# Performance work log

Measured on AMD Instinct MI355X. Metric: run time of the kernel, lower is better.

## Reference

```python
import jax, jax.numpy as jnp
import numpy as np

N_NODES = 100000
N_EDGES = 3200000
N_FEAT = 16
N_GRAPHS = 1024


def setup_inputs() -> dict:
    key = jax.random.key(0)
    ks = jax.random.split(key, 12)
    x = jax.random.normal(ks[0], (N_NODES, N_FEAT), dtype=jnp.float32)
    edge_index = jax.random.randint(ks[1], (2, N_EDGES), 0, N_NODES, dtype=jnp.int32)
    batch = jnp.sort(jax.random.randint(ks[2], (N_NODES,), 0, N_GRAPHS, dtype=jnp.int32))
    def lin(k, fan_in, fan_out):
        s = 1.0 / np.sqrt(fan_in)
        return jax.random.uniform(k, (fan_in, fan_out), jnp.float32, -s, s)
    W1 = lin(ks[3], N_FEAT, 64); b1 = jnp.zeros((64,), jnp.float32)
    W2 = lin(ks[4], 64, 32);     b2 = jnp.zeros((32,), jnp.float32)
    fc1_W = lin(ks[5], 32, 16);  fc1_b = jnp.zeros((16,), jnp.float32)
    fc2_W = lin(ks[6], 16, 1);   fc2_b = jnp.zeros((1,), jnp.float32)
    return {"x": x, "edge_index": edge_index, "batch": batch,
            "W1": W1, "b1": b1, "W2": W2, "b2": b2,
            "fc1_W": fc1_W, "fc1_b": fc1_b, "fc2_W": fc2_W, "fc2_b": fc2_b}


def _gcn_conv(h, W, b, src, dst, norm, n_nodes):
    # h: [N, Fin] -> [N, Fout]; symmetric-normalized scatter-add (PyG GCNConv)
    h = h @ W
    msg = h[src] * norm[:, None]            # edge-wise gather + scale
    out = jax.ops.segment_sum(msg, dst, num_segments=n_nodes)
    return out + b


def reference(x, edge_index, batch, W1, b1, W2, b2, fc1_W, fc1_b, fc2_W, fc2_b):
    n_nodes = x.shape[0]
    # add self-loops
    loops = jnp.arange(n_nodes, dtype=edge_index.dtype)
    src = jnp.concatenate([edge_index[0], loops])
    dst = jnp.concatenate([edge_index[1], loops])
    deg = jax.ops.segment_sum(jnp.ones_like(dst, dtype=x.dtype), dst, num_segments=n_nodes)
    dinv = jnp.where(deg > 0, jax.lax.rsqrt(deg), 0.0)
    norm = dinv[src] * dinv[dst]

    h = jax.nn.relu(_gcn_conv(x, W1, b1, src, dst, norm, n_nodes))
    # dropout p=0.2 is identity at inference
    h = jax.nn.relu(_gcn_conv(h, W2, b2, src, dst, norm, n_nodes))

    # global mean pool over graphs
    sums = jax.ops.segment_sum(h, batch, num_segments=N_GRAPHS)
    cnts = jax.ops.segment_sum(jnp.ones((n_nodes,), h.dtype), batch, num_segments=N_GRAPHS)
    g = sums / jnp.maximum(cnts, 1.0)[:, None]

    g = jax.nn.relu(g @ fc1_W + fc1_b)
    # dropout p=0.5 is identity at inference
    out = g @ fc2_W + fc2_b
    return jax.nn.sigmoid(out)  # [N_GRAPHS, 1]
```

## Files before the change

### kernel.cpp

```cpp
#include <hip/hip_runtime.h>
#include <math.h>

#define NNODES  100000
#define NEDGES  3200000
#define NGRAPHS 1024
#define BNODES  196
#define NBUCK   ((NNODES + BNODES - 1) / BNODES)
#define SCAP    8192
#define PADCAP  10240
#define SLDS    7168
#define DUMMY   NNODES
#define CHUNK   4096
#define NCHUNKS ((NEDGES + CHUNK - 1) / CHUNK)

typedef int iv4 __attribute__((ext_vector_type(4)));
typedef float fv2 __attribute__((ext_vector_type(2)));

#if defined(__has_builtin)
#if __has_builtin(__builtin_amdgcn_cvt_pk_f32_fp8) && __has_builtin(__builtin_amdgcn_cvt_pk_fp8_f32)
#define HW_FP8 1
#endif
#endif

__device__ __forceinline__ unsigned bf16pair(float a, float b) {
    unsigned ua = __float_as_uint(a), ub = __float_as_uint(b);
    ua += 0x7fffu + ((ua >> 16) & 1u);
    ub += 0x7fffu + ((ub >> 16) & 1u);
    return (ua >> 16) | (ub & 0xffff0000u);
}
__device__ __forceinline__ float bflo(unsigned u) { return __uint_as_float(u << 16); }
__device__ __forceinline__ float bfhi(unsigned u) { return __uint_as_float(u & 0xffff0000u); }

__device__ __forceinline__ unsigned fp8_of(float v) {
    unsigned s = (__float_as_uint(v) >> 24) & 0x80u;
    float a = fminf(fabsf(v), 448.f);
    unsigned ub = __float_as_uint(a);
    unsigned lsb = (ub >> 20) & 1u;
    ub += 0x0007FFFFu + lsb;
    int em = (int)(ub >> 20) - (120 << 3);
    if (em < 1) return s;
    if (em > 0x7E) em = 0x7E;
    return s | (unsigned)em;
}
__device__ __forceinline__ float fp8_to_f(unsigned b) {
    unsigned em = b & 0x7Fu;
    unsigned s = (b & 0x80u) << 24;
    float f = __uint_as_float(s | ((em + 0x3C0u) << 20));
    return (em >= 8u) ? f : 0.f;
}
__device__ __forceinline__ unsigned fp8x4_pack(float a, float b, float c, float d) {
    a = fminf(fmaxf(a, -448.f), 448.f);
    b = fminf(fmaxf(b, -448.f), 448.f);
    c = fminf(fmaxf(c, -448.f), 448.f);
    d = fminf(fmaxf(d, -448.f), 448.f);
#ifdef HW_FP8
    int w = __builtin_amdgcn_cvt_pk_fp8_f32(a, b, 0, false);
    w = __builtin_amdgcn_cvt_pk_fp8_f32(c, d, w, true);
    return (unsigned)w;
#else
    return fp8_of(a) | (fp8_of(b) << 8) | (fp8_of(c) << 16) | (fp8_of(d) << 24);
#endif
}
__device__ __forceinline__ fv2 f8lo(unsigned w) {
#ifdef HW_FP8
    return __builtin_amdgcn_cvt_pk_f32_fp8((int)w, false);
#else
    fv2 t; t.x = fp8_to_f(w & 0xFFu); t.y = fp8_to_f((w >> 8) & 0xFFu); return t;
#endif
}
__device__ __forceinline__ fv2 f8hi(unsigned w) {
#ifdef HW_FP8
    return __builtin_amdgcn_cvt_pk_f32_fp8((int)w, true);
#else
    fv2 t; t.x = fp8_to_f((w >> 16) & 0xFFu); t.y = fp8_to_f(w >> 24); return t;
#endif
}


__global__ void zero4_kernel(int4* p, int nvec) {
    int i = blockIdx.x * blockDim.x + threadIdx.x;
    if (i < nvec) p[i] = make_int4(0, 0, 0, 0);
}


__global__ void binA_kernel(const int* __restrict__ src, const int* __restrict__ dst,
                            int* __restrict__ bucketCur, int* __restrict__ stage) {
    __shared__ int lcnt[NBUCK + 1];
    __shared__ int boff[NBUCK + 1];
    __shared__ int gbase[NBUCK + 1];
    __shared__ int cur[NBUCK + 1];
    __shared__ int wtot[4];
    __shared__ int packed[CHUNK];
    __shared__ unsigned short bof[CHUNK];
    int tid = threadIdx.x;
    int beg = blockIdx.x * CHUNK;
    int end = beg + CHUNK; if (end > NEDGES) end = NEDGES;
    int cnt = end - beg;

    for (int i = tid; i <= NBUCK; i += 256) lcnt[i] = 0;
    __syncthreads();

    int ent[16];
    int bk[16];
#pragma unroll
    for (int it = 0; it < 4; ++it) {
        int e0 = beg + tid * 4 + it * 1024;
        if (e0 < end) {
            iv4 d4 = __builtin_nontemporal_load((const iv4*)(dst + e0));
            iv4 s4 = __builtin_nontemporal_load((const iv4*)(src + e0));
            int b;
            b = d4.x / BNODES; ent[it*4+0] = s4.x | ((d4.x - b*BNODES) << 17); bk[it*4+0] = b; atomicAdd(&lcnt[b], 1);
            b = d4.y / BNODES; ent[it*4+1] = s4.y | ((d4.y - b*BNODES) << 17); bk[it*4+1] = b; atomicAdd(&lcnt[b], 1);
            b = d4.z / BNODES; ent[it*4+2] = s4.z | ((d4.z - b*BNODES) << 17); bk[it*4+2] = b; atomicAdd(&lcnt[b], 1);
            b = d4.w / BNODES; ent[it*4+3] = s4.w | ((d4.w - b*BNODES) << 17); bk[it*4+3] = b; atomicAdd(&lcnt[b], 1);
        } else {
            bk[it*4+0] = -1; bk[it*4+1] = -1; bk[it*4+2] = -1; bk[it*4+3] = -1;
            ent[it*4+0] = 0; ent[it*4+1] = 0; ent[it*4+2] = 0; ent[it*4+3] = 0;
        }
    }
    __syncthreads();

    int b0 = 2 * tid, b1 = 2 * tid + 1;
    int c0 = lcnt[b0];
    int c1 = (b1 < NBUCK) ? lcnt[b1] : 0;
    int sum = c0 + c1;
    int lane = tid & 63, wid = tid >> 6;
    int v = sum;
#pragma unroll
    for (int o = 1; o < 64; o <<= 1) {
        int t = __shfl_up(v, o, 64);
        if (lane >= o) v += t;
    }
    if (lane == 63) wtot[wid] = v;
    __syncthreads();
    int woff = 0;
#pragma unroll
    for (int w = 0; w < 4; ++w) woff += (w < wid) ? wtot[w] : 0;
    int excl = woff + v - sum;
    boff[b0] = excl; cur[b0] = excl;
    if (b1 < NBUCK) { boff[b1] = excl + c0; cur[b1] = excl + c0; }
    if (c0 > 0) gbase[b0] = atomicAdd(&bucketCur[b0], c0);
    if (b1 < NBUCK && c1 > 0) gbase[b1] = atomicAdd(&bucketCur[b1], c1);
    __syncthreads();

#pragma unroll
    for (int k = 0; k < 16; ++k) {
        int b = bk[k];
        if (b >= 0) {
            int p = atomicAdd(&cur[b], 1);
            packed[p] = ent[k];
            bof[p] = (unsigned short)b;
        }
    }
    __syncthreads();

    for (int i = tid; i < cnt; i += 256) {
        int b = bof[i];
        int addr = b * SCAP + gbase[b] + (i - boff[b]);
        stage[addr] = packed[i];
    }
}


__global__ void binB_kernel(const int* __restrict__ bucketCur,
                            const int* __restrict__ stage, const float2* __restrict__ x,
                            int* __restrict__ entries, int* __restrict__ rowptr,
                            int* __restrict__ rowend,
                            float* __restrict__ dinv, unsigned* __restrict__ xs) {
    __shared__ int s[256];
    __shared__ int ncur[256];
    __shared__ float ndinv[256];
    __shared__ int wt[4];
    __shared__ int se[SLDS];
    int b = blockIdx.x;
    int cntE = bucketCur[b];
    int bbase = b * PADCAP;
    int nlo = b * BNODES;
    int nn = NNODES - nlo; if (nn > BNODES) nn = BNODES;
    int sb = b * SCAP;
    int tid = threadIdx.x;

    s[tid] = 0;
    __syncthreads();
    for (int e = tid; e < cntE; e += 256) {
        int w = stage[sb + e];
        if (e < SLDS) se[e] = w;
        atomicAdd(&s[(unsigned)w >> 17], 1);
    }
    __syncthreads();
    int v = s[tid];
    int p16 = (v + 15) & ~15;
    int lane = tid & 63, wid = tid >> 6;
    int iv = p16;
#pragma unroll
    for (int o = 1; o < 64; o <<= 1) {
        int t = __shfl_up(iv, o, 64);
        if (lane >= o) iv += t;
    }
    if (lane == 63) wt[wid] = iv;
    __syncthreads();
    int woff = 0;
#pragma unroll
    for (int w2 = 0; w2 < 4; ++w2) woff += (w2 < wid) ? wt[w2] : 0;
    int pexcl = woff + iv - p16;
    ncur[tid] = pexcl;
    if (tid < nn) {
        rowptr[nlo + tid] = bbase + pexcl;
        rowend[nlo + tid] = bbase + pexcl + p16;
        float di = rsqrtf((float)(v + 1));
        dinv[nlo + tid] = di;
        ndinv[tid] = di;
    }
    __syncthreads();
    for (int i = tid; i < nn * 8; i += 256) {
        int node = i >> 3, w = i & 7;
        float2 v2 = x[(size_t)(nlo + node) * 8 + w];
        float di = ndinv[node];
        xs[(nlo + node) * 8 + w] = bf16pair(v2.x * di, v2.y * di);
    }
    if (b == NBUCK - 1) {
        for (int i = tid; i < 8; i += 256) xs[NNODES * 8 + i] = 0u;
    }
    if (tid < nn) {
        int base = bbase + pexcl;
        for (int j = v; j < p16; ++j) entries[base + j] = DUMMY;
    }
    for (int e = tid; e < cntE; e += 256) {
        unsigned w = (unsigned)((e < SLDS) ? se[e] : stage[sb + e]);
        int dl = (int)(w >> 17);
        int slot = atomicAdd(&ncur[dl], 1);
        entries[bbase + slot] = (int)(w & 0x1FFFFu);
    }
}


__device__ __forceinline__ void acc_bf(unsigned u, fv2& a) {
    fv2 t; t.x = bflo(u); t.y = bfhi(u);
    a += t;
}
#define ACCX4(V) { acc_bf((V).x, acc0); acc_bf((V).y, acc1); acc_bf((V).z, acc2); acc_bf((V).w, acc3); }
#define QRED(a) { a.x += __shfl_xor(a.x, 2); a.y += __shfl_xor(a.y, 2); \
                  a.x += __shfl_xor(a.x, 4); a.y += __shfl_xor(a.y, 4); }

__global__ void __launch_bounds__(256) gatherX_mlp_kernel(const int* __restrict__ entries,
        const int* __restrict__ rowptr, const int* __restrict__ rowend,
        const float* __restrict__ dinv, const uint4* __restrict__ xsv,
        const float* __restrict__ W1, const float* __restrict__ b1,
        const float* __restrict__ W2, unsigned* __restrict__ hm2f) {
    __shared__ __align__(16) float w1s[16 * 64];
    __shared__ __align__(16) float w2s[64 * 32];
    __shared__ float bb1[64];
    int tid = threadIdx.x;
    for (int i = tid; i < 16 * 64; i += 256) w1s[i] = W1[i];
    for (int i = tid; i < 64 * 32; i += 256) w2s[i] = W2[i];
    if (tid < 64) bb1[tid] = b1[tid];
    if (blockIdx.x == 0 && tid < 8) hm2f[NNODES * 8 + tid] = 0u;
    __syncthreads();

    int t = blockIdx.x * 256 + tid;
    int n = t >> 3, lane = t & 7;
    int half = lane & 1, quad = lane >> 1;
    int beg = rowptr[n];
    int nb = (rowend[n] - beg) >> 4;
    fv2 acc0 = {0.f, 0.f}, acc1 = {0.f, 0.f}, acc2 = {0.f, 0.f}, acc3 = {0.f, 0.f};
    if (quad == 0) {
        uint4 sv = xsv[n * 2 + half];
        ACCX4(sv);
    }

    const int* ep = entries + beg + (quad << 2);
    if (nb > 0) {
        uint4 p0, p1, p2, p3;
        iv4 enx = {0, 0, 0, 0};
        {
            iv4 e; __builtin_memcpy(&e, ep, 16);
            p0 = xsv[e.x * 2 + half]; p1 = xsv[e.y * 2 + half];
            p2 = xsv[e.z * 2 + half]; p3 = xsv[e.w * 2 + half];
            if (nb > 1) __builtin_memcpy(&enx, ep + 16, 16);
        }
        for (int i = 1; i < nb; ++i) {
            uint4 c0 = xsv[enx.x * 2 + half], c1 = xsv[enx.y * 2 + half],
                  c2 = xsv[enx.z * 2 + half], c3 = xsv[enx.w * 2 + half];
            if (i + 1 < nb) __builtin_memcpy(&enx, ep + ((i + 1) << 4), 16);
            ACCX4(p0); ACCX4(p1); ACCX4(p2); ACCX4(p3);
            p0 = c0; p1 = c1; p2 = c2; p3 = c3;
        }
        ACCX4(p0); ACCX4(p1); ACCX4(p2); ACCX4(p3);
    }

    QRED(acc0); QRED(acc1); QRED(acc2); QRED(acc3);

    float di = dinv[n];
    float own[8];
    own[0] = acc0.x * di; own[1] = acc0.y * di; own[2] = acc1.x * di; own[3] = acc1.y * di;
    own[4] = acc2.x * di; own[5] = acc2.y * di; own[6] = acc3.x * di; own[7] = acc3.y * di;
    float oth[8];
#pragma unroll
    for (int i2 = 0; i2 < 8; ++i2) oth[i2] = __shfl_xor(own[i2], 1);
    float a16[16];
#pragma unroll
    for (int k = 0; k < 8; ++k) a16[k]     = (half == 0) ? own[k] : oth[k];
#pragma unroll
    for (int k = 0; k < 8; ++k) a16[8 + k] = (half == 0) ? oth[k] : own[k];

    float h[8];
    {
        int j0 = lane * 8;
#pragma unroll
        for (int jj = 0; jj < 8; ++jj) h[jj] = bb1[j0 + jj];
#pragma unroll
        for (int k = 0; k < 16; ++k) {
            const float4* wr = (const float4*)(w1s + k * 64 + j0);
            float4 wa = wr[0], wb = wr[1];
            float av = a16[k];
            h[0] += av * wa.x; h[1] += av * wa.y; h[2] += av * wa.z; h[3] += av * wa.w;
            h[4] += av * wb.x; h[5] += av * wb.y; h[6] += av * wb.z; h[7] += av * wb.w;
        }
#pragma unroll
        for (int jj = 0; jj < 8; ++jj) h[jj] = fmaxf(h[jj], 0.f);
    }

    {
        int j0c = lane * 4;
        float c0 = 0.f, c1 = 0.f, c2 = 0.f, c3 = 0.f;
#pragma unroll
        for (int k = 0; k < 64; ++k) {
            float hv = __shfl(h[k & 7], k >> 3, 8);
            float4 w = *(const float4*)(w2s + k * 32 + j0c);
            c0 += hv * w.x; c1 += hv * w.y; c2 += hv * w.z; c3 += hv * w.w;
        }
        float sc = di * 64.f;
        hm2f[n * 8 + lane] = fp8x4_pack(c0 * sc, c1 * sc, c2 * sc, c3 * sc);
    }
}


#define ACCH4(V) { q0lo += f8lo((V).x); q0hi += f8hi((V).x); \
                   q1lo += f8lo((V).y); q1hi += f8hi((V).y); \
                   q2lo += f8lo((V).z); q2hi += f8hi((V).z); \
                   q3lo += f8lo((V).w); q3hi += f8hi((V).w); }

__global__ void __launch_bounds__(256) gatherH_pool_kernel(const int* __restrict__ entries,
        const int* __restrict__ rowptr, const int* __restrict__ rowend,
        const float* __restrict__ dinv, const uint4* __restrict__ hm4,
        const float4* __restrict__ b2, const int* __restrict__ batch,
        float* __restrict__ psum, float* __restrict__ pcnt) {
    __shared__ float lps[8][32];
    __shared__ float lpc[8];
    int tid = threadIdx.x;
    ((float*)lps)[tid] = 0.f;
    if (tid < 8) lpc[tid] = 0.f;
    __syncthreads();

    int t = blockIdx.x * 256 + tid;
    int n = t >> 3, lane = t & 7;
    int half = lane & 1, quad = lane >> 1;
    int g0 = batch[blockIdx.x * 32];
    int beg = rowptr[n];
    int nb = (rowend[n] - beg) >> 4;
    fv2 q0lo = {0.f,0.f}, q0hi = {0.f,0.f}, q1lo = {0.f,0.f}, q1hi = {0.f,0.f},
        q2lo = {0.f,0.f}, q2hi = {0.f,0.f}, q3lo = {0.f,0.f}, q3hi = {0.f,0.f};
    if (quad == 0) {
        uint4 sv = hm4[n * 2 + half];
        ACCH4(sv);
    }

    const int* ep = entries + beg + (quad << 2);
    if (nb > 0) {
        uint4 p0, p1, p2, p3;
        iv4 enx = {0, 0, 0, 0};
        {
            iv4 e; __builtin_memcpy(&e, ep, 16);
            p0 = hm4[e.x * 2 + half]; p1 = hm4[e.y * 2 + half];
            p2 = hm4[e.z * 2 + half]; p3 = hm4[e.w * 2 + half];
            if (nb > 1) __builtin_memcpy(&enx, ep + 16, 16);
        }
        for (int i = 1; i < nb; ++i) {
            uint4 c0 = hm4[enx.x * 2 + half], c1 = hm4[enx.y * 2 + half],
                  c2 = hm4[enx.z * 2 + half], c3 = hm4[enx.w * 2 + half];
            if (i + 1 < nb) __builtin_memcpy(&enx, ep + ((i + 1) << 4), 16);
            ACCH4(p0); ACCH4(p1); ACCH4(p2); ACCH4(p3);
            p0 = c0; p1 = c1; p2 = c2; p3 = c3;
        }
        ACCH4(p0); ACCH4(p1); ACCH4(p2); ACCH4(p3);
    }

    QRED(q0lo); QRED(q0hi); QRED(q1lo); QRED(q1hi);
    QRED(q2lo); QRED(q2hi); QRED(q3lo); QRED(q3hi);

    if (quad == 0) {
        float sc = dinv[n] * (1.0f / 64.f);
        float4 bv0 = b2[half * 4 + 0], bv1 = b2[half * 4 + 1],
               bv2 = b2[half * 4 + 2], bv3 = b2[half * 4 + 3];
        float vv[16];
        vv[0]  = fmaxf(q0lo.x * sc + bv0.x, 0.f);
        vv[1]  = fmaxf(q0lo.y * sc + bv0.y, 0.f);
        vv[2]  = fmaxf(q0hi.x * sc + bv0.z, 0.f);
        vv[3]  = fmaxf(q0hi.y * sc + bv0.w, 0.f);
        vv[4]  = fmaxf(q1lo.x * sc + bv1.x, 0.f);
        vv[5]  = fmaxf(q1lo.y * sc + bv1.y, 0.f);
        vv[6]  = fmaxf(q1hi.x * sc + bv1.z, 0.f);
        vv[7]  = fmaxf(q1hi.y * sc + bv1.w, 0.f);
        vv[8]  = fmaxf(q2lo.x * sc + bv2.x, 0.f);
        vv[9]  = fmaxf(q2lo.y * sc + bv2.y, 0.f);
        vv[10] = fmaxf(q2hi.x * sc + bv2.z, 0.f);
        vv[11] = fmaxf(q2hi.y * sc + bv2.w, 0.f);
        vv[12] = fmaxf(q3lo.x * sc + bv3.x, 0.f);
        vv[13] = fmaxf(q3lo.y * sc + bv3.y, 0.f);
        vv[14] = fmaxf(q3hi.x * sc + bv3.z, 0.f);
        vv[15] = fmaxf(q3hi.y * sc + bv3.w, 0.f);

        int g = batch[n], gr = g - g0;
        if (gr < 8) {
            float* pg = &lps[gr][half * 16];
#pragma unroll
            for (int k2 = 0; k2 < 16; ++k2) atomicAdd(pg + k2, vv[k2]);
            if (lane == 0) atomicAdd(&lpc[gr], 1.0f);
        } else {
            float* pg = psum + g * 32 + half * 16;
#pragma unroll
            for (int k2 = 0; k2 < 16; ++k2) atomicAdd(pg + k2, vv[k2]);
            if (lane == 0) atomicAdd(&pcnt[g], 1.0f);
        }
    }
    __syncthreads();
    int grf = tid >> 5, f = tid & 31;
    float v = lps[grf][f];
    if (v != 0.f) atomicAdd(&psum[(g0 + grf) * 32 + f], v);
    if (f == 0) {
        float c = lpc[grf];
        if (c != 0.f) atomicAdd(&pcnt[g0 + grf], c);
    }
}


__global__ void head_kernel(const float* __restrict__ psum, const float* __restrict__ pcnt,
                            const float* __restrict__ fc1W, const float* __restrict__ fc1b,
                            const float* __restrict__ fc2W, const float* __restrict__ fc2b,
                            float* __restrict__ out) {
    int g = blockIdx.x * blockDim.x + threadIdx.x;
    if (g >= NGRAPHS) return;
    float inv = 1.0f / fmaxf(pcnt[g], 1.0f);
    float gv[32];
#pragma unroll
    for (int k = 0; k < 32; ++k) gv[k] = psum[g * 32 + k] * inv;
    float o = fc2b[0];
#pragma unroll
    for (int j = 0; j < 16; ++j) {
        float h = fc1b[j];
#pragma unroll
        for (int k = 0; k < 32; ++k) h += gv[k] * fc1W[k * 16 + j];
        h = fmaxf(h, 0.f);
        o += h * fc2W[j];
    }
    out[g] = 1.0f / (1.0f + expf(-o));
}


extern "C" void kernel_launch(void* const* d_in, const int* in_sizes, int n_in,
                              void* d_out, int out_size, void* d_ws, size_t ws_size,
                              hipStream_t stream) {
    const float* x    = (const float*)d_in[0];
    const int*   ei   = (const int*)d_in[1];
    const int*   batch= (const int*)d_in[2];
    const float* W1   = (const float*)d_in[3];
    const float* b1   = (const float*)d_in[4];
    const float* W2   = (const float*)d_in[5];
    const float* b2   = (const float*)d_in[6];
    const float* fc1W = (const float*)d_in[7];
    const float* fc1b = (const float*)d_in[8];
    const float* fc2W = (const float*)d_in[9];
    const float* fc2b = (const float*)d_in[10];
    float* out = (float*)d_out;

    const int* src = ei;
    const int* dst = ei + NEDGES;

    char* wsb = (char*)d_ws;
    int*      bucketCur = (int*)wsb;
    float*    psum      = (float*)(wsb + 2048);
    float*    pcnt      = (float*)(wsb + 133120);
    float*    dinv      = (float*)(wsb + 137216);
    int*      rowptr    = (int*)(wsb + 537216);
    int*      rowend    = (int*)(wsb + 937216);
    int*      stage     = (int*)(wsb + 1337216);
    int*      entries   = (int*)(wsb + 18081664);
    unsigned* xs        = (unsigned*)(wsb + 39012224);
    unsigned* hm2f      = (unsigned*)(wsb + 42212256);

    const int B = 256;
    zero4_kernel<<<(8576 + B - 1) / B, B, 0, stream>>>((int4*)wsb, 8576);

    binA_kernel<<<NCHUNKS, B, 0, stream>>>(src, dst, bucketCur, stage);
    binB_kernel<<<NBUCK, B, 0, stream>>>(bucketCur, stage, (const float2*)x,
                                         entries, rowptr, rowend, dinv, xs);

    const int GTH = NNODES * 8 / B;
    gatherX_mlp_kernel<<<GTH, B, 0, stream>>>(entries, rowptr, rowend, dinv,
                                              (const uint4*)xs, W1, b1, W2, hm2f);
    gatherH_pool_kernel<<<GTH, B, 0, stream>>>(entries, rowptr, rowend, dinv,
                                               (const uint4*)hm2f, (const float4*)b2,
                                               batch, psum, pcnt);
    head_kernel<<<(NGRAPHS + B - 1) / B, B, 0, stream>>>(psum, pcnt, fc1W, fc1b, fc2W, fc2b, out);
}
```

Measured before the change: 231.0 us.

## Halve bucket size and split bucket counters into sub-buckets to cut atomic contention

Buckets now cover 98 nodes instead of 196, giving about 1021 buckets. Each bucket's staging area is split into 4 sub-buckets selected by chunk index, which spreads the global atomicAdd traffic on bucket counters across more addresses. binB then gathers the four sub-regions into LDS, which removes the global-memory fallback for oversized buckets. The cost is more binB blocks doing less work each, with half the threads idle in the per-node phase, and a fixed 1024-entry sub-bucket capacity that could overflow on skewed inputs.

```diff
diff --git a/kernel.cpp b/kernel.cpp
--- a/kernel.cpp
+++ b/kernel.cpp
@@ -4,11 +4,11 @@
 #define NNODES  100000
 #define NEDGES  3200000
 #define NGRAPHS 1024
-#define BNODES  196
+#define BNODES  98
 #define NBUCK   ((NNODES + BNODES - 1) / BNODES)
-#define SCAP    8192
-#define PADCAP  10240
-#define SLDS    7168
+#define NSUB    4
+#define SUBCAP  1024
+#define PADCAP  5120
 #define DUMMY   NNODES
 #define CHUNK   4096
 #define NCHUNKS ((NEDGES + CHUNK - 1) / CHUNK)
@@ -85,19 +85,20 @@
 
 __global__ void binA_kernel(const int* __restrict__ src, const int* __restrict__ dst,
                             int* __restrict__ bucketCur, int* __restrict__ stage) {
-    __shared__ int lcnt[NBUCK + 1];
-    __shared__ int boff[NBUCK + 1];
-    __shared__ int gbase[NBUCK + 1];
-    __shared__ int cur[NBUCK + 1];
+    __shared__ int lcnt[1024];
+    __shared__ int boff[1024];
+    __shared__ int gbase[1024];
+    __shared__ int cur[1024];
     __shared__ int wtot[4];
     __shared__ int packed[CHUNK];
     __shared__ unsigned short bof[CHUNK];
     int tid = threadIdx.x;
+    int sub = blockIdx.x & (NSUB - 1);
     int beg = blockIdx.x * CHUNK;
     int end = beg + CHUNK; if (end > NEDGES) end = NEDGES;
     int cnt = end - beg;
 
-    for (int i = tid; i <= NBUCK; i += 256) lcnt[i] = 0;
+    for (int i = tid; i < 1024; i += 256) lcnt[i] = 0;
     __syncthreads();
 
     int ent[16];
@@ -120,10 +121,9 @@
     }
     __syncthreads();
 
-    int b0 = 2 * tid, b1 = 2 * tid + 1;
-    int c0 = lcnt[b0];
-    int c1 = (b1 < NBUCK) ? lcnt[b1] : 0;
-    int sum = c0 + c1;
+    int q0 = 4 * tid;
+    int c0 = lcnt[q0], c1 = lcnt[q0 + 1], c2 = lcnt[q0 + 2], c3 = lcnt[q0 + 3];
+    int sum = c0 + c1 + c2 + c3;
     int lane = tid & 63, wid = tid >> 6;
     int v = sum;
 #pragma unroll
@@ -137,10 +137,14 @@
 #pragma unroll
     for (int w = 0; w < 4; ++w) woff += (w < wid) ? wtot[w] : 0;
     int excl = woff + v - sum;
-    boff[b0] = excl; cur[b0] = excl;
-    if (b1 < NBUCK) { boff[b1] = excl + c0; cur[b1] = excl + c0; }
-    if (c0 > 0) gbase[b0] = atomicAdd(&bucketCur[b0], c0);
-    if (b1 < NBUCK && c1 > 0) gbase[b1] = atomicAdd(&bucketCur[b1], c1);
+    boff[q0] = excl;     cur[q0] = excl;     excl += c0;
+    boff[q0 + 1] = excl; cur[q0 + 1] = excl; excl += c1;
+    boff[q0 + 2] = excl; cur[q0 + 2] = excl; excl += c2;
+    boff[q0 + 3] = excl; cur[q0 + 3] = excl;
+    if (c0 > 0) gbase[q0]     = atomicAdd(&bucketCur[q0 * NSUB + sub], c0);
+    if (c1 > 0) gbase[q0 + 1] = atomicAdd(&bucketCur[(q0 + 1) * NSUB + sub], c1);
+    if (c2 > 0) gbase[q0 + 2] = atomicAdd(&bucketCur[(q0 + 2) * NSUB + sub], c2);
+    if (c3 > 0) gbase[q0 + 3] = atomicAdd(&bucketCur[(q0 + 3) * NSUB + sub], c3);
     __syncthreads();
 
 #pragma unroll
@@ -156,7 +160,7 @@
 
     for (int i = tid; i < cnt; i += 256) {
         int b = bof[i];
-        int addr = b * SCAP + gbase[b] + (i - boff[b]);
+        int addr = (b * NSUB + sub) * SUBCAP + gbase[b] + (i - boff[b]);
         stage[addr] = packed[i];
     }
 }
@@ -167,49 +171,59 @@
                             int* __restrict__ entries, int* __restrict__ rowptr,
                             int* __restrict__ rowend,
                             float* __restrict__ dinv, unsigned* __restrict__ xs) {
-    __shared__ int s[256];
-    __shared__ int ncur[256];
-    __shared__ float ndinv[256];
-    __shared__ int wt[4];
-    __shared__ int se[SLDS];
+    __shared__ int s[128];
+    __shared__ int ncur[128];
+    __shared__ float ndinv[128];
+    __shared__ int wt[2];
+    __shared__ int se[NSUB * SUBCAP];
     int b = blockIdx.x;
-    int cntE = bucketCur[b];
+    int tid = threadIdx.x;
+    int c0 = bucketCur[b * NSUB + 0], c1 = bucketCur[b * NSUB + 1];
+    int c2 = bucketCur[b * NSUB + 2], c3 = bucketCur[b * NSUB + 3];
+    int o1 = c0, o2 = c0 + c1, o3 = o2 + c2;
+    int cntE = o3 + c3;
     int bbase = b * PADCAP;
     int nlo = b * BNODES;
     int nn = NNODES - nlo; if (nn > BNODES) nn = BNODES;
-    int sb = b * SCAP;
-    int tid = threadIdx.x;
-
-    s[tid] = 0;
-    __syncthreads();
-    for (int e = tid; e < cntE; e += 256) {
-        int w = stage[sb + e];
-        if (e < SLDS) se[e] = w;
-        atomicAdd(&s[(unsigned)w >> 17], 1);
-    }
-    __syncthreads();
-    int v = s[tid];
-    int p16 = (v + 15) & ~15;
+
+    if (tid < 128) s[tid] = 0;
+    __syncthreads();
+    {
+        const int* sp = stage + b * (NSUB * SUBCAP);
+        for (int e = tid; e < c0; e += 256) { int w = sp[e];              se[e]      = w; atomicAdd(&s[(unsigned)w >> 17], 1); }
+        for (int e = tid; e < c1; e += 256) { int w = sp[SUBCAP + e];     se[o1 + e] = w; atomicAdd(&s[(unsigned)w >> 17], 1); }
+        for (int e = tid; e < c2; e += 256) { int w = sp[2 * SUBCAP + e]; se[o2 + e] = w; atomicAdd(&s[(unsigned)w >> 17], 1); }
+        for (int e = tid; e < c3; e += 256) { int w = sp[3 * SUBCAP + e]; se[o3 + e] = w; atomicAdd(&s[(unsigned)w >> 17], 1); }
+    }
+    __syncthreads();
+
+    int v = 0, p16 = 0, iv = 0;
     int lane = tid & 63, wid = tid >> 6;
-    int iv = p16;
-#pragma unroll
-    for (int o = 1; o < 64; o <<= 1) {
-        int t = __shfl_up(iv, o, 64);
-        if (lane >= o) iv += t;
-    }
-    if (lane == 63) wt[wid] = iv;
-    __syncthreads();
-    int woff = 0;
-#pragma unroll
-    for (int w2 = 0; w2 < 4; ++w2) woff += (w2 < wid) ? wt[w2] : 0;
-    int pexcl = woff + iv - p16;
-    ncur[tid] = pexcl;
-    if (tid < nn) {
-        rowptr[nlo + tid] = bbase + pexcl;
-        rowend[nlo + tid] = bbase + pexcl + p16;
-        float di = rsqrtf((float)(v + 1));
-        dinv[nlo + tid] = di;
-        ndinv[tid] = di;
+    if (tid < 128) {
+        v = s[tid];
+        p16 = (v + 15) & ~15;
+        iv = p16;
+#pragma unroll
+        for (int o = 1; o < 64; o <<= 1) {
+            int t = __shfl_up(iv, o, 64);
+            if (lane >= o) iv += t;
+        }
+        if (lane == 63) wt[wid] = iv;
+    }
+    __syncthreads();
+    if (tid < 128) {
+        int woff = (wid == 1) ? wt[0] : 0;
+        int pexcl = woff + iv - p16;
+        ncur[tid] = pexcl;
+        if (tid < nn) {
+            rowptr[nlo + tid] = bbase + pexcl;
+            rowend[nlo + tid] = bbase + pexcl + p16;
+            float di = rsqrtf((float)(v + 1));
+            dinv[nlo + tid] = di;
+            ndinv[tid] = di;
+            int base = bbase + pexcl;
+            for (int j = v; j < p16; ++j) entries[base + j] = DUMMY;
+        }
     }
     __syncthreads();
     for (int i = tid; i < nn * 8; i += 256) {
@@ -221,12 +235,8 @@
     if (b == NBUCK - 1) {
         for (int i = tid; i < 8; i += 256) xs[NNODES * 8 + i] = 0u;
     }
-    if (tid < nn) {
-        int base = bbase + pexcl;
-        for (int j = v; j < p16; ++j) entries[base + j] = DUMMY;
-    }
     for (int e = tid; e < cntE; e += 256) {
-        unsigned w = (unsigned)((e < SLDS) ? se[e] : stage[sb + e]);
+        unsigned w = (unsigned)se[e];
         int dl = (int)(w >> 17);
         int slot = atomicAdd(&ncur[dl], 1);
         entries[bbase + slot] = (int)(w & 0x1FFFFu);
@@ -478,18 +488,18 @@
 
     char* wsb = (char*)d_ws;
     int*      bucketCur = (int*)wsb;
-    float*    psum      = (float*)(wsb + 2048);
-    float*    pcnt      = (float*)(wsb + 133120);
-    float*    dinv      = (float*)(wsb + 137216);
-    int*      rowptr    = (int*)(wsb + 537216);
-    int*      rowend    = (int*)(wsb + 937216);
-    int*      stage     = (int*)(wsb + 1337216);
-    int*      entries   = (int*)(wsb + 18081664);
-    unsigned* xs        = (unsigned*)(wsb + 39012224);
-    unsigned* hm2f      = (unsigned*)(wsb + 42212256);
+    float*    psum      = (float*)(wsb + 16384);
+    float*    pcnt      = (float*)(wsb + 147456);
+    float*    dinv      = (float*)(wsb + 151552);
+    int*      rowptr    = (int*)(wsb + 551552);
+    int*      rowend    = (int*)(wsb + 951552);
+    int*      stage     = (int*)(wsb + 1351552);
+    int*      entries   = (int*)(wsb + 18079616);
+    unsigned* xs        = (unsigned*)(wsb + 38989696);
+    unsigned* hm2f      = (unsigned*)(wsb + 42189728);
 
     const int B = 256;
-    zero4_kernel<<<(8576 + B - 1) / B, B, 0, stream>>>((int4*)wsb, 8576);
+    zero4_kernel<<<(9472 + B - 1) / B, B, 0, stream>>>((int4*)wsb, 9472);
 
     binA_kernel<<<NCHUNKS, B, 0, stream>>>(src, dst, bucketCur, stage);
     binB_kernel<<<NBUCK, B, 0, stream>>>(bucketCur, stage, (const float2*)x,
```

Measured after the change: 258.9 us. 12.1% more time.
